# Kernel optimization log

Measured on AMD Instinct MI355X. Metric: run time of the kernel, lower is better.

The kernel has to match this reference:

```python
import jax, jax.numpy as jnp
import numpy as np

B, L, D, N = 2, 2048, 1024, 16
DT_MIN, DT_MAX = 1e-3, 1e-1


def setup_inputs() -> dict:
    key = jax.random.key(0)
    ks = jax.random.split(key, 8)
    u = jax.random.normal(ks[0], (B, L, D), dtype=jnp.float32)
    # torch.nn.Linear weights are (out_features, in_features)
    W_dt = jax.random.normal(ks[1], (D, D), dtype=jnp.float32) * 0.02
    b_dt = jnp.zeros((D,), dtype=jnp.float32)
    W_B = jax.random.normal(ks[2], (D * N, D), dtype=jnp.float32) * 0.02
    b_B = jnp.zeros((D * N,), dtype=jnp.float32)
    W_C = jax.random.normal(ks[3], (D * N, D), dtype=jnp.float32) * 0.02
    b_C = jnp.zeros((D * N,), dtype=jnp.float32)
    # log_A init: log(1..N) broadcast over channels (HiPPO-ish diagonal)
    log_A = jnp.broadcast_to(jnp.log(jnp.arange(1, N + 1, dtype=jnp.float32)), (D, N))
    D_skip = jnp.ones((D,), dtype=jnp.float32)
    lo, hi = float(np.log(DT_MIN)), float(np.log(DT_MAX))
    dt_bias = jax.random.uniform(ks[4], (D,), dtype=jnp.float32) * (hi - lo) + lo
    return {"u": u, "log_A": log_A, "D_skip": D_skip, "dt_bias": dt_bias,
            "W_dt": W_dt, "b_dt": b_dt, "W_B": W_B, "b_B": b_B,
            "W_C": W_C, "b_C": b_C}


def reference(u, log_A, D_skip, dt_bias, W_dt, b_dt, W_B, b_B, W_C, b_C):
    b, l, d = u.shape
    n = log_A.shape[1]
    A = -jnp.exp(log_A)                                   # (d, n), A < 0
    # token-dependent parameters, computed for all timesteps at once
    dt = jax.nn.softplus(u @ W_dt.T + b_dt + dt_bias)     # (b, l, d)
    Bt = (u @ W_B.T + b_B).reshape(b, l, d, n)            # (b, l, d, n)
    Ct = (u @ W_C.T + b_C).reshape(b, l, d, n)            # (b, l, d, n)
    # exact ZOH discretisation
    A_bar = jnp.exp(dt[..., None] * A)                    # (b, l, d, n)
    B_bar = (A_bar - 1.0) / A * Bt                        # (b, l, d, n)
    x_in = B_bar * u[..., None]                           # (b, l, d, n)
    # recurrent scan over time
    def step(h, inp):
        a_t, x_t, c_t = inp                               # each (b, d, n)
        h = a_t * h + x_t
        y_t = jnp.sum(c_t * h, axis=-1)                   # (b, d)
        return h, y_t
    h0 = jnp.zeros((b, d, n), dtype=u.dtype)
    xs = (jnp.moveaxis(A_bar, 1, 0), jnp.moveaxis(x_in, 1, 0), jnp.moveaxis(Ct, 1, 0))
    _, ys = jax.lax.scan(step, h0, xs)                    # ys: (l, b, d)
    y = jnp.moveaxis(ys, 0, 1) + D_skip * u               # (b, l, d)
    return y
```

## Files before the change

kernel.cpp:

```cpp
#include <hip/hip_runtime.h>
#include <hip/hip_bf16.h>
#include <stdint.h>

constexpr int Bb = 2;
constexpr int Ll = 2048;
constexpr int Dd = 1024;
constexpr int Nn = 16;
constexpr int NB = Dd * Nn;
constexpr int SL = 64;
constexpr int NCH = Bb * Dd;
constexpr int KCAT = 3 * Dd;

typedef __bf16 bf16_t;
typedef __bf16 bf16x8 __attribute__((ext_vector_type(8)));
typedef __bf16 bf16x4 __attribute__((ext_vector_type(4)));
typedef float f32x4 __attribute__((ext_vector_type(4)));

__device__ inline void gld_lds16(const void* g, void* l) {
    __builtin_amdgcn_global_load_lds(
        (const __attribute__((address_space(1))) unsigned int*)g,
        (__attribute__((address_space(3))) unsigned int*)l, 16, 0, 0);
}

__global__ __launch_bounds__(256) void cvt_bf16(const float* __restrict__ s,
                                                bf16_t* __restrict__ d, int n4) {
    int i = blockIdx.x * 256 + threadIdx.x;
    const int stride = gridDim.x * 256;
    const float4* s4 = (const float4*)s;
    bf16x4* d4 = (bf16x4*)d;
    for (; i < n4; i += stride) {
        float4 v = s4[i];
        bf16x4 o = {(bf16_t)v.x, (bf16_t)v.y, (bf16_t)v.z, (bf16_t)v.w};
        d4[i] = o;
    }
}

__global__ __launch_bounds__(256) void build_ucat(const float* __restrict__ u,
                                                  bf16_t* __restrict__ ucat,
                                                  bf16_t* __restrict__ ubf) {
    const int i = blockIdx.x * 256 + threadIdx.x;
    const int row = i >> 8;
    const int c = (i & 255) << 2;
    float4 v = ((const float4*)u)[i];
    bf16x4 hi = {(bf16_t)v.x, (bf16_t)v.y, (bf16_t)v.z, (bf16_t)v.w};
    bf16x4 lo = {(bf16_t)(v.x - (float)hi.x), (bf16_t)(v.y - (float)hi.y),
                 (bf16_t)(v.z - (float)hi.z), (bf16_t)(v.w - (float)hi.w)};
    bf16_t* r = ucat + (size_t)row * KCAT;
    *(bf16x4*)(r + c) = hi;
    *(bf16x4*)(r + Dd + c) = lo;
    *(bf16x4*)(r + 2 * Dd + c) = hi;
    *(bf16x4*)(ubf + (size_t)i * 4) = hi;
}

__global__ __launch_bounds__(256) void build_wcat(const float* __restrict__ w,
                                                  bf16_t* __restrict__ wcat) {
    const int i = blockIdx.x * 256 + threadIdx.x;
    const int row = i >> 8;
    const int c = (i & 255) << 2;
    float4 v = ((const float4*)w)[i];
    bf16x4 hi = {(bf16_t)v.x, (bf16_t)v.y, (bf16_t)v.z, (bf16_t)v.w};
    bf16x4 lo = {(bf16_t)(v.x - (float)hi.x), (bf16_t)(v.y - (float)hi.y),
                 (bf16_t)(v.z - (float)hi.z), (bf16_t)(v.w - (float)hi.w)};
    bf16_t* r = wcat + (size_t)row * KCAT;
    *(bf16x4*)(r + c) = hi;
    *(bf16x4*)(r + Dd + c) = hi;
    *(bf16x4*)(r + 2 * Dd + c) = lo;
}

template <int EP, typename OutT>
__global__ __launch_bounds__(256) void gemm_mfma(
    const bf16_t* __restrict__ Abase, int CL, int l0, int K,
    const bf16_t* __restrict__ W, const float* __restrict__ b1,
    const float* __restrict__ b2, OutT* __restrict__ C, int N)
{
    __shared__ bf16_t As[128 * 32];
    __shared__ bf16_t Bs[128 * 32];

    const int tid = threadIdx.x;
    const int bn = blockIdx.x * 128;
    const int rglob = blockIdx.y * 128;
    const int batch = rglob / CL;
    const int rin = rglob % CL;
    const bf16_t* Ap = Abase + ((size_t)batch * Ll + l0 + rin) * K;
    const bf16_t* Wp = W + (size_t)bn * K;
    OutT* Cp = C + (size_t)rglob * N;

    const int sr = tid >> 2;
    const int sc = (tid & 3) << 3;
    char* ldsA = (char*)As + tid * 16;
    char* ldsB = (char*)Bs + tid * 16;

    const int lane = tid & 63;
    const int wid = tid >> 6;
    const int wm = (wid & 1) << 6;
    const int wn = (wid >> 1) << 6;
    const int lr = lane & 15;
    const int lq = lane >> 4;

    f32x4 acc[4][4] = {};

    for (int k0 = 0; k0 < K; k0 += 32) {
        __syncthreads();
        gld_lds16(Ap + (size_t)sr * K + k0 + sc, ldsA);
        gld_lds16(Ap + (size_t)(sr + 64) * K + k0 + sc, ldsA + 4096);
        gld_lds16(Wp + (size_t)sr * K + k0 + sc, ldsB);
        gld_lds16(Wp + (size_t)(sr + 64) * K + k0 + sc, ldsB + 4096);
        __syncthreads();

        bf16x8 af[4], bfr[4];
#pragma unroll
        for (int mi = 0; mi < 4; ++mi)
            af[mi] = *(const bf16x8*)&As[(wm + mi * 16 + lr) * 32 + lq * 8];
#pragma unroll
        for (int ni = 0; ni < 4; ++ni)
            bfr[ni] = *(const bf16x8*)&Bs[(wn + ni * 16 + lr) * 32 + lq * 8];
#pragma unroll
        for (int mi = 0; mi < 4; ++mi)
#pragma unroll
            for (int ni = 0; ni < 4; ++ni)
                acc[mi][ni] = __builtin_amdgcn_mfma_f32_16x16x32_bf16(
                    af[mi], bfr[ni], acc[mi][ni], 0, 0, 0);
    }

#pragma unroll
    for (int ni = 0; ni < 4; ++ni) {
        const int col = bn + wn + ni * 16 + lr;
        const float bc = b1[col] + (EP == 1 ? b2[col] : 0.f);
#pragma unroll
        for (int mi = 0; mi < 4; ++mi)
#pragma unroll
            for (int i = 0; i < 4; ++i) {
                float v = acc[mi][ni][i] + bc;
                if (EP == 1) v = (v > 20.f) ? v : log1pf(__expf(v));
                Cp[(size_t)(wm + mi * 16 + lq * 4 + i) * N + col] = (OutT)v;
            }
    }
}

__global__ __launch_bounds__(512, 4) void gemm_dt(
    const bf16_t* __restrict__ A, int K, const bf16_t* __restrict__ W,
    const float* __restrict__ b1, const float* __restrict__ b2,
    float* __restrict__ C)
{
    extern __shared__ char smem[];
    char* const smA = smem;
    char* const smB = smem + 49152;
    const int tid = threadIdx.x;
    const int bn = blockIdx.x * 128;
    const int row0 = blockIdx.y * 128;
    const bf16_t* Ap = A + (size_t)row0 * K;
    const bf16_t* Wp = W + (size_t)bn * K;
    float* Cp = C + (size_t)row0 * Dd;

    const int lane = tid & 63;
    const int wid = tid >> 6;
    const int wr = wid >> 2;
    const int wc = wid & 3;
    const int lr = lane & 15;
    const int lq = lane >> 4;
    const int NT = K >> 6;

    const int c0 = tid, c1 = tid + 512;
    const int r0 = c0 >> 3, r1 = c1 >> 3;
    const int kb0 = ((c0 & 7) << 3) ^ ((r0 & 7) << 3);
    const int kb1 = ((c1 & 7) << 3) ^ ((r1 & 7) << 3);

    auto stageA = [&](int tt, int slot) {
        gld_lds16(Ap + (size_t)r0 * K + tt * 64 + kb0, smA + slot * 16384 + c0 * 16);
        gld_lds16(Ap + (size_t)r1 * K + tt * 64 + kb1, smA + slot * 16384 + c1 * 16);
    };
    auto stageB = [&](int tt, int slot) {
        gld_lds16(Wp + (size_t)r0 * K + tt * 64 + kb0, smB + slot * 16384 + c0 * 16);
        gld_lds16(Wp + (size_t)r1 * K + tt * 64 + kb1, smB + slot * 16384 + c1 * 16);
    };

    stageA(0, 0); stageB(0, 0); stageA(1, 1); stageB(1, 1);
    asm volatile("s_waitcnt vmcnt(4)" ::: "memory");
    __builtin_amdgcn_s_barrier();

    f32x4 acc[4][2] = {};
    const int xsw = (lr & 7) << 4;
    int as_rd = 0, as_wr = 2;

    for (int t = 0; t < NT; ++t) {
        const char* Ard = smA + as_rd * 16384;
        const char* Brd = smB + (t & 1) * 16384;

        bf16x8 bfr[2][2];
#pragma unroll
        for (int p = 0; p < 4; ++p) {
            if (p == 0 && t + 2 < NT) stageA(t + 2, as_wr);
            if (p == 2 && t + 2 < NT) stageB(t + 2, (t & 1));

            if (p == 0) {
#pragma unroll
                for (int ks = 0; ks < 2; ++ks)
#pragma unroll
                    for (int ni = 0; ni < 2; ++ni)
                        bfr[ks][ni] = *(const bf16x8*)(Brd +
                            (wc * 32 + ni * 16 + lr) * 128 +
                            ((ks * 64 + lq * 16) ^ xsw));
            }
            bf16x8 ak0 = *(const bf16x8*)(Ard +
                (wr * 64 + p * 16 + lr) * 128 + ((lq * 16) ^ xsw));
            bf16x8 ak1 = *(const bf16x8*)(Ard +
                (wr * 64 + p * 16 + lr) * 128 + ((64 + lq * 16) ^ xsw));

            __builtin_amdgcn_s_barrier();
            __builtin_amdgcn_s_setprio(1);
#pragma unroll
            for (int ni = 0; ni < 2; ++ni) {
                acc[p][ni] = __builtin_amdgcn_mfma_f32_16x16x32_bf16(
                    bfr[0][ni], ak0, acc[p][ni], 0, 0, 0);
                acc[p][ni] = __builtin_amdgcn_mfma_f32_16x16x32_bf16(
                    bfr[1][ni], ak1, acc[p][ni], 0, 0, 0);
            }
            __builtin_amdgcn_s_setprio(0);
            if (p == 3) {
                if (t + 2 < NT)
                    asm volatile("s_waitcnt vmcnt(4)" ::: "memory");
                else if (t + 1 < NT)
                    asm volatile("s_waitcnt vmcnt(0)" ::: "memory");
            }
            __builtin_amdgcn_s_barrier();
        }
        ++as_rd; if (as_rd == 3) as_rd = 0;
        ++as_wr; if (as_wr == 3) as_wr = 0;
    }

#pragma unroll
    for (int ni = 0; ni < 2; ++ni) {
        const int col = bn + wc * 32 + ni * 16 + lq * 4;
        const float4 ba = *(const float4*)&b1[col];
        const float4 bb = *(const float4*)&b2[col];
        const float bc[4] = {ba.x + bb.x, ba.y + bb.y, ba.z + bb.z, ba.w + bb.w};
#pragma unroll
        for (int mi = 0; mi < 4; ++mi) {
            const int row = wr * 64 + mi * 16 + lr;
            f32x4 v;
#pragma unroll
            for (int i = 0; i < 4; ++i) {
                float tv = acc[mi][ni][i] + bc[i];
                v[i] = (tv > 20.f) ? tv : log1pf(__expf(tv));
            }
            *(f32x4*)(Cp + (size_t)row * Dd + col) = v;
        }
    }
}

__global__ __launch_bounds__(512, 2) void gemm256_bc(
    const bf16_t* __restrict__ Abase, int CL, int l0, int K,
    const bf16_t* __restrict__ WB, const bf16_t* __restrict__ WC,
    const float* __restrict__ bB, const float* __restrict__ bC,
    bf16_t* __restrict__ OB, bf16_t* __restrict__ OC)
{
    extern __shared__ char smem[];
    char* const smA = smem;
    char* const smB = smem + 98304;
    const int tid = threadIdx.x;

    const int NY = (2 * CL) >> 8;
    const int id = blockIdx.x;
    const int cx = id & 7;
    const int jj = id >> 3;
    const int x = cx * 16 + jj / NY;
    const int yb = jj % NY;

    const int rglob = yb * 256;
    const int batch = rglob / CL;
    const int rin = rglob % CL;
    const bf16_t* Ap = Abase + ((size_t)batch * Ll + l0 + rin) * K;

    const bf16_t* Wp; const float* bias; bf16_t* Co; int bn;
    if (x < 64) { Wp = WB; bias = bB; Co = OB; bn = x * 256; }
    else        { Wp = WC; bias = bC; Co = OC; bn = (x - 64) * 256; }
    Wp += (size_t)bn * K;
    bf16_t* Cp = Co + (size_t)rglob * NB;

    const int lane = tid & 63;
    const int wid = tid >> 6;
    const int wr = wid >> 2;
    const int wc = wid & 3;
    const int lr = lane & 15;
    const int lq = lane >> 4;
    const int NT = K >> 6;

    const int c0 = tid, c1 = tid + 512;
    const int r0 = c0 >> 3, r1 = c1 >> 3;
    const int kb0 = ((c0 & 7) << 3) ^ ((r0 & 7) << 3);
    const int kb1 = ((c1 & 7) << 3) ^ ((r1 & 7) << 3);

    auto stageA = [&](int tt, int slot, int h) {
        gld_lds16(Ap + (size_t)(h * 128 + r0) * K + tt * 64 + kb0,
                  smA + slot * 32768 + h * 16384 + c0 * 16);
        gld_lds16(Ap + (size_t)(h * 128 + r1) * K + tt * 64 + kb1,
                  smA + slot * 32768 + h * 16384 + c1 * 16);
    };
    auto stageB = [&](int tt, int slot, int h) {
        gld_lds16(Wp + (size_t)(h * 128 + r0) * K + tt * 64 + kb0,
                  smB + slot * 32768 + h * 16384 + c0 * 16);
        gld_lds16(Wp + (size_t)(h * 128 + r1) * K + tt * 64 + kb1,
                  smB + slot * 32768 + h * 16384 + c1 * 16);
    };

    stageB(0, 0, 0); stageB(0, 0, 1);
    stageA(0, 0, 0); stageA(0, 0, 1);
    stageA(1, 1, 0); stageA(1, 1, 1);
    asm volatile("s_waitcnt vmcnt(4)" ::: "memory");
    __builtin_amdgcn_s_barrier();

    f32x4 acc[8][4] = {};
    const int xsw = (lr & 7) << 4;
    int as_rd = 0, as_wr = 2;

    for (int t = 0; t < NT; ++t) {
        const char* Ard = smA + as_rd * 32768;
        const char* Brd = smB + (t & 1) * 32768;

        if (t + 1 < NT) { stageB(t + 1, (t + 1) & 1, 0); stageB(t + 1, (t + 1) & 1, 1); }
        if (t + 2 < NT) { stageA(t + 2, as_wr, 0); stageA(t + 2, as_wr, 1); }

        bf16x8 bfr[2][4];
#pragma unroll
        for (int ks = 0; ks < 2; ++ks)
#pragma unroll
            for (int ni = 0; ni < 4; ++ni)
                bfr[ks][ni] = *(const bf16x8*)(Brd +
                    (wc * 64 + ni * 16 + lr) * 128 +
                    ((ks * 64 + lq * 16) ^ xsw));

#pragma unroll
        for (int p = 0; p < 4; ++p) {
            bf16x8 a0k0 = *(const bf16x8*)(Ard +
                (wr * 128 + (2 * p) * 16 + lr) * 128 + ((lq * 16) ^ xsw));
            bf16x8 a0k1 = *(const bf16x8*)(Ard +
                (wr * 128 + (2 * p) * 16 + lr) * 128 + ((64 + lq * 16) ^ xsw));
            bf16x8 a1k0 = *(const bf16x8*)(Ard +
                (wr * 128 + (2 * p + 1) * 16 + lr) * 128 + ((lq * 16) ^ xsw));
            bf16x8 a1k1 = *(const bf16x8*)(Ard +
                (wr * 128 + (2 * p + 1) * 16 + lr) * 128 + ((64 + lq * 16) ^ xsw));
#pragma unroll
            for (int ni = 0; ni < 4; ++ni) {
                acc[2 * p][ni] = __builtin_amdgcn_mfma_f32_16x16x32_bf16(
                    bfr[0][ni], a0k0, acc[2 * p][ni], 0, 0, 0);
                acc[2 * p][ni] = __builtin_amdgcn_mfma_f32_16x16x32_bf16(
                    bfr[1][ni], a0k1, acc[2 * p][ni], 0, 0, 0);
                acc[2 * p + 1][ni] = __builtin_amdgcn_mfma_f32_16x16x32_bf16(
                    bfr[0][ni], a1k0, acc[2 * p + 1][ni], 0, 0, 0);
                acc[2 * p + 1][ni] = __builtin_amdgcn_mfma_f32_16x16x32_bf16(
                    bfr[1][ni], a1k1, acc[2 * p + 1][ni], 0, 0, 0);
            }
        }

        if (t + 2 < NT)
            asm volatile("s_waitcnt vmcnt(4)" ::: "memory");
        else if (t + 1 < NT)
            asm volatile("s_waitcnt vmcnt(0)" ::: "memory");
        __builtin_amdgcn_s_barrier();

        ++as_rd; if (as_rd == 3) as_rd = 0;
        ++as_wr; if (as_wr == 3) as_wr = 0;
    }

    float4 bv[4];
#pragma unroll
    for (int ni = 0; ni < 4; ++ni)
        bv[ni] = *(const float4*)&bias[bn + wc * 64 + ni * 16 + lq * 4];
#pragma unroll
    for (int mi = 0; mi < 8; ++mi) {
        const size_t rowoff = (size_t)(wr * 128 + mi * 16 + lr) * NB;
#pragma unroll
        for (int ni = 0; ni < 4; ++ni) {
            const int col = bn + wc * 64 + ni * 16 + lq * 4;
            bf16x4 o = {(bf16_t)(acc[mi][ni][0] + bv[ni].x),
                        (bf16_t)(acc[mi][ni][1] + bv[ni].y),
                        (bf16_t)(acc[mi][ni][2] + bv[ni].z),
                        (bf16_t)(acc[mi][ni][3] + bv[ni].w)};
            *(bf16x4*)(Cp + rowoff + col) = o;
        }
    }
}

__global__ __launch_bounds__(256) void scan_seg_local(
    const float* __restrict__ u, const float* __restrict__ dt,
    const bf16_t* __restrict__ Bt_c, const float* __restrict__ log_A,
    float* __restrict__ pseg, float* __restrict__ hseg, int CL, int l0)
{
    const int tid = threadIdx.x;
    const int g = tid >> 4, n = tid & 15;
    const int gid = blockIdx.x * 16 + g;
    const int ch = gid & (NCH - 1);
    const int s = gid >> 11;
    const int b = ch >> 10, d = ch & (Dd - 1);

    const float A = -__expf(log_A[d * Nn + n]);
    const float rA = 1.f / A;

    size_t idx_bn = (size_t)(b * CL + s * SL) * NB + d * Nn + n;
    size_t idx_u = ((size_t)b * Ll + l0 + s * SL) * Dd + d;

    float p = 1.f, h = 0.f;
    for (int l = 0; l < SL; ++l) {
        const float dtv = dt[idx_u];
        const float uv = u[idx_u];
        const float bv = (float)Bt_c[idx_bn];
        const float a = __expf(dtv * A);
        p *= a;
        h = a * h + (a - 1.f) * rA * bv * uv;
        idx_bn += NB; idx_u += Dd;
    }
    const size_t o = ((size_t)s * NCH + ch) * Nn + n;
    pseg[o] = p;
    hseg[o] = h;
}

__global__ __launch_bounds__(256) void scan_combine(
    const float* __restrict__ pseg, const float* __restrict__ hseg,
    float* __restrict__ hin_arr, float* __restrict__ h_state,
    int NSEG, int l0)
{
    const int t = blockIdx.x * 256 + threadIdx.x;
    float hin = (l0 == 0) ? 0.f : h_state[t];
    for (int s = 0; s < NSEG; ++s) {
        const size_t o = (size_t)s * (NCH * Nn) + t;
        hin_arr[o] = hin;
        hin = pseg[o] * hin + hseg[o];
    }
    h_state[t] = hin;
}

__global__ __launch_bounds__(256) void scan_seg_final(
    const float* __restrict__ u, const float* __restrict__ dt,
    const bf16_t* __restrict__ Bt_c, const bf16_t* __restrict__ Ct_c,
    const float* __restrict__ log_A, const float* __restrict__ D_skip,
    const float* __restrict__ hin_arr, float* __restrict__ y, int CL, int l0)
{
    const int tid = threadIdx.x;
    const int g = tid >> 4, n = tid & 15;
    const int gid = blockIdx.x * 16 + g;
    const int ch = gid & (NCH - 1);
    const int s = gid >> 11;
    const int b = ch >> 10, d = ch & (Dd - 1);

    const float A = -__expf(log_A[d * Nn + n]);
    const float rA = 1.f / A;
    const float Dsk = D_skip[d];

    size_t idx_bn = (size_t)(b * CL + s * SL) * NB + d * Nn + n;
    size_t idx_u = ((size_t)b * Ll + l0 + s * SL) * Dd + d;

    float h = hin_arr[((size_t)s * NCH + ch) * Nn + n];
    for (int l = 0; l < SL; ++l) {
        const float dtv = dt[idx_u];
        const float uv = u[idx_u];
        const float bv = (float)Bt_c[idx_bn];
        const float cv = (float)Ct_c[idx_bn];
        const float a = __expf(dtv * A);
        h = a * h + (a - 1.f) * rA * bv * uv;
        float p = cv * h;
        p += __shfl_xor(p, 1);
        p += __shfl_xor(p, 2);
        p += __shfl_xor(p, 4);
        p += __shfl_xor(p, 8);
        if (n == 0) y[idx_u] = p + Dsk * uv;
        idx_bn += NB; idx_u += Dd;
    }
}

static inline size_t al256(size_t x) { return (x + 255) & ~(size_t)255; }

extern "C" void kernel_launch(void* const* d_in, const int* in_sizes, int n_in,
                              void* d_out, int out_size, void* d_ws, size_t ws_size,
                              hipStream_t stream) {
    const float* u       = (const float*)d_in[0];
    const float* log_A   = (const float*)d_in[1];
    const float* D_skip  = (const float*)d_in[2];
    const float* dt_bias = (const float*)d_in[3];
    const float* W_dt    = (const float*)d_in[4];
    const float* b_dt    = (const float*)d_in[5];
    const float* W_B     = (const float*)d_in[6];
    const float* b_B     = (const float*)d_in[7];
    const float* W_C     = (const float*)d_in[8];
    const float* b_C     = (const float*)d_in[9];
    float* y = (float*)d_out;

    hipFuncSetAttribute(reinterpret_cast<const void*>(gemm256_bc),
                        hipFuncAttributeMaxDynamicSharedMemorySize, 163840);
    hipFuncSetAttribute(reinterpret_cast<const void*>(gemm_dt),
                        hipFuncAttributeMaxDynamicSharedMemorySize, 81920);

    const size_t sz_ubf  = al256((size_t)Bb * Ll * Dd * 2);
    const size_t sz_w    = al256((size_t)NB * Dd * 2);
    const size_t sz_h    = al256((size_t)NCH * Nn * 4);
    const size_t sz_dtf  = al256((size_t)Bb * Ll * Dd * 4);
    const size_t sz_ucat = al256((size_t)Bb * Ll * KCAT * 2);
    const size_t sz_wcat = al256((size_t)Dd * KCAT * 2);

    int CL = 128;
    const int cands[5] = {2048, 1024, 512, 256, 128};
    for (int i = 0; i < 5; ++i) {
        const int c = cands[i];
        const int nseg = c / SL;
        const size_t seg = 3 * al256((size_t)nseg * NCH * Nn * 4);
        const size_t chunk = 2 * al256((size_t)2 * c * NB * 2);
        const size_t ovl = sz_ucat + sz_wcat;
        const size_t need = sz_ubf + 2 * sz_w + sz_h + sz_dtf + seg +
                            (chunk > ovl ? chunk : ovl);
        if (need <= ws_size) { CL = c; break; }
    }
    const int NSEG = CL / SL;

    char* p = (char*)d_ws;
    bf16_t* u_bf   = (bf16_t*)p; p += sz_ubf;
    bf16_t* wB_bf  = (bf16_t*)p; p += sz_w;
    bf16_t* wC_bf  = (bf16_t*)p; p += sz_w;
    float* h_state = (float*)p; p += sz_h;
    float* dt_full = (float*)p; p += sz_dtf;
    const size_t sz_seg1 = al256((size_t)NSEG * NCH * Nn * 4);
    float* pseg    = (float*)p; p += sz_seg1;
    float* hseg    = (float*)p; p += sz_seg1;
    float* hin_arr = (float*)p; p += sz_seg1;
    char* chunk0 = p;
    bf16_t* Bt_c = (bf16_t*)chunk0;
    bf16_t* Ct_c = (bf16_t*)(chunk0 + al256((size_t)2 * CL * NB * 2));
    bf16_t* u_cat = (bf16_t*)chunk0;
    bf16_t* w_cat = (bf16_t*)(chunk0 + sz_ucat);

    cvt_bf16<<<2048, 256, 0, stream>>>(W_B, wB_bf, NB * Dd / 4);
    cvt_bf16<<<2048, 256, 0, stream>>>(W_C, wC_bf, NB * Dd / 4);
    build_ucat<<<Bb * Ll * Dd / 4 / 256, 256, 0, stream>>>(u, u_cat, u_bf);
    build_wcat<<<Dd * Dd / 4 / 256, 256, 0, stream>>>(W_dt, w_cat);

    gemm_dt<<<dim3(Dd / 128, Bb * Ll / 128), 512, 81920, stream>>>(
        u_cat, KCAT, w_cat, b_dt, dt_bias, dt_full);

    const bool use256 = (CL % 256 == 0);
    for (int l0 = 0; l0 < Ll; l0 += CL) {
        if (use256) {
            const int NY = 2 * CL / 256;
            gemm256_bc<<<dim3(128 * NY), 512, 163840, stream>>>(
                u_bf, CL, l0, Dd, wB_bf, wC_bf, b_B, b_C, Bt_c, Ct_c);
        } else {
            gemm_mfma<0, bf16_t><<<dim3(NB / 128, 2 * CL / 128), 256, 0, stream>>>(
                u_bf, CL, l0, Dd, wB_bf, b_B, nullptr, Bt_c, NB);
            gemm_mfma<0, bf16_t><<<dim3(NB / 128, 2 * CL / 128), 256, 0, stream>>>(
                u_bf, CL, l0, Dd, wC_bf, b_C, nullptr, Ct_c, NB);
        }
        scan_seg_local<<<dim3(128 * NSEG), 256, 0, stream>>>(
            u, dt_full, Bt_c, log_A, pseg, hseg, CL, l0);
        scan_combine<<<dim3(128), 256, 0, stream>>>(
            pseg, hseg, hin_arr, h_state, NSEG, l0);
        scan_seg_final<<<dim3(128 * NSEG), 256, 0, stream>>>(
            u, dt_full, Bt_c, Ct_c, log_A, D_skip, hin_arr, y, CL, l0);
    }
}
```

Before: 686.1 us.

## Fuse prep kernels, switch B/C GEMM to 32x32 MFMA, fold scan combine into final

Merges the four bf16 conversion and concat kernels into one grid-stride prep kernel to cut launch count. Rewrites the inner loop of the 256-tile B/C GEMM to use 32x32x16 bf16 MFMA instructions with fewer fragment loads per K step. It also removes the separate scan_combine kernel: each final-scan block recomputes its incoming state by serially chaining the earlier segment summaries, with a ping-pong h_state buffer across chunks. The trade is redundant prefix work per segment in exchange for fewer launches and less intermediate memory.

After: 709.9 us. 3.5% more time.

```diff
diff --git a/kernel.cpp b/kernel.cpp
--- a/kernel.cpp
+++ b/kernel.cpp
@@ -15,6 +15,7 @@
 typedef __bf16 bf16x8 __attribute__((ext_vector_type(8)));
 typedef __bf16 bf16x4 __attribute__((ext_vector_type(4)));
 typedef float f32x4 __attribute__((ext_vector_type(4)));
+typedef float f32x16 __attribute__((ext_vector_type(16)));
 
 __device__ inline void gld_lds16(const void* g, void* l) {
     __builtin_amdgcn_global_load_lds(
@@ -22,49 +23,53 @@
         (__attribute__((address_space(3))) unsigned int*)l, 16, 0, 0);
 }
 
-__global__ __launch_bounds__(256) void cvt_bf16(const float* __restrict__ s,
-                                                bf16_t* __restrict__ d, int n4) {
+__global__ __launch_bounds__(256) void prep_all(
+    const float* __restrict__ u, const float* __restrict__ W_B,
+    const float* __restrict__ W_C, const float* __restrict__ W_dt,
+    bf16_t* __restrict__ wB_bf, bf16_t* __restrict__ wC_bf,
+    bf16_t* __restrict__ ucat, bf16_t* __restrict__ ubf,
+    bf16_t* __restrict__ wcat)
+{
+    constexpr int NW = NB * Dd / 4;
+    constexpr int NU = Bb * Ll * Dd / 4;
+    constexpr int NWc = Dd * Dd / 4;
+    constexpr int TOT = 2 * NW + NU + NWc;
     int i = blockIdx.x * 256 + threadIdx.x;
     const int stride = gridDim.x * 256;
-    const float4* s4 = (const float4*)s;
-    bf16x4* d4 = (bf16x4*)d;
-    for (; i < n4; i += stride) {
-        float4 v = s4[i];
-        bf16x4 o = {(bf16_t)v.x, (bf16_t)v.y, (bf16_t)v.z, (bf16_t)v.w};
-        d4[i] = o;
-    }
-}
-
-__global__ __launch_bounds__(256) void build_ucat(const float* __restrict__ u,
-                                                  bf16_t* __restrict__ ucat,
-                                                  bf16_t* __restrict__ ubf) {
-    const int i = blockIdx.x * 256 + threadIdx.x;
-    const int row = i >> 8;
-    const int c = (i & 255) << 2;
-    float4 v = ((const float4*)u)[i];
-    bf16x4 hi = {(bf16_t)v.x, (bf16_t)v.y, (bf16_t)v.z, (bf16_t)v.w};
-    bf16x4 lo = {(bf16_t)(v.x - (float)hi.x), (bf16_t)(v.y - (float)hi.y),
-                 (bf16_t)(v.z - (float)hi.z), (bf16_t)(v.w - (float)hi.w)};
-    bf16_t* r = ucat + (size_t)row * KCAT;
-    *(bf16x4*)(r + c) = hi;
-    *(bf16x4*)(r + Dd + c) = lo;
-    *(bf16x4*)(r + 2 * Dd + c) = hi;
-    *(bf16x4*)(ubf + (size_t)i * 4) = hi;
-}
-
-__global__ __launch_bounds__(256) void build_wcat(const float* __restrict__ w,
-                                                  bf16_t* __restrict__ wcat) {
-    const int i = blockIdx.x * 256 + threadIdx.x;
-    const int row = i >> 8;
-    const int c = (i & 255) << 2;
-    float4 v = ((const float4*)w)[i];
-    bf16x4 hi = {(bf16_t)v.x, (bf16_t)v.y, (bf16_t)v.z, (bf16_t)v.w};
-    bf16x4 lo = {(bf16_t)(v.x - (float)hi.x), (bf16_t)(v.y - (float)hi.y),
-                 (bf16_t)(v.z - (float)hi.z), (bf16_t)(v.w - (float)hi.w)};
-    bf16_t* r = wcat + (size_t)row * KCAT;
-    *(bf16x4*)(r + c) = hi;
-    *(bf16x4*)(r + Dd + c) = hi;
-    *(bf16x4*)(r + 2 * Dd + c) = lo;
+    for (; i < TOT; i += stride) {
+        if (i < 2 * NW) {
+            const float4 v = (i < NW) ? ((const float4*)W_B)[i]
+                                      : ((const float4*)W_C)[i - NW];
+            bf16x4 o = {(bf16_t)v.x, (bf16_t)v.y, (bf16_t)v.z, (bf16_t)v.w};
+            if (i < NW) ((bf16x4*)wB_bf)[i] = o;
+            else        ((bf16x4*)wC_bf)[i - NW] = o;
+        } else if (i < 2 * NW + NU) {
+            const int j = i - 2 * NW;
+            const int row = j >> 8;
+            const int c = (j & 255) << 2;
+            float4 v = ((const float4*)u)[j];
+            bf16x4 hi = {(bf16_t)v.x, (bf16_t)v.y, (bf16_t)v.z, (bf16_t)v.w};
+            bf16x4 lo = {(bf16_t)(v.x - (float)hi.x), (bf16_t)(v.y - (float)hi.y),
+                         (bf16_t)(v.z - (float)hi.z), (bf16_t)(v.w - (float)hi.w)};
+            bf16_t* r = ucat + (size_t)row * KCAT;
+            *(bf16x4*)(r + c) = hi;
+            *(bf16x4*)(r + Dd + c) = lo;
+            *(bf16x4*)(r + 2 * Dd + c) = hi;
+            *(bf16x4*)(ubf + (size_t)j * 4) = hi;
+        } else {
+            const int j = i - 2 * NW - NU;
+            const int row = j >> 8;
+            const int c = (j & 255) << 2;
+            float4 v = ((const float4*)W_dt)[j];
+            bf16x4 hi = {(bf16_t)v.x, (bf16_t)v.y, (bf16_t)v.z, (bf16_t)v.w};
+            bf16x4 lo = {(bf16_t)(v.x - (float)hi.x), (bf16_t)(v.y - (float)hi.y),
+                         (bf16_t)(v.z - (float)hi.z), (bf16_t)(v.w - (float)hi.w)};
+            bf16_t* r = wcat + (size_t)row * KCAT;
+            *(bf16x4*)(r + c) = hi;
+            *(bf16x4*)(r + Dd + c) = hi;
+            *(bf16x4*)(r + 2 * Dd + c) = lo;
+        }
+    }
 }
 
 template <int EP, typename OutT>
@@ -281,8 +286,8 @@
     const int wid = tid >> 6;
     const int wr = wid >> 2;
     const int wc = wid & 3;
-    const int lr = lane & 15;
-    const int lq = lane >> 4;
+    const int lr5 = lane & 31;
+    const int hq = lane >> 5;
     const int NT = K >> 6;
 
     const int c0 = tid, c1 = tid + 512;
@@ -309,9 +314,11 @@
     asm volatile("s_waitcnt vmcnt(4)" ::: "memory");
     __builtin_amdgcn_s_barrier();
 
-    f32x4 acc[8][4] = {};
-    const int xsw = (lr & 7) << 4;
+    f32x16 acc[4][2] = {};
     int as_rd = 0, as_wr = 2;
+
+    const int arow = wr * 128 + lr5;
+    const int brow = wc * 64 + lr5;
 
     for (int t = 0; t < NT; ++t) {
         const char* Ard = smA + as_rd * 32768;
@@ -320,36 +327,26 @@
         if (t + 1 < NT) { stageB(t + 1, (t + 1) & 1, 0); stageB(t + 1, (t + 1) & 1, 1); }
         if (t + 2 < NT) { stageA(t + 2, as_wr, 0); stageA(t + 2, as_wr, 1); }
 
-        bf16x8 bfr[2][4];
-#pragma unroll
-        for (int ks = 0; ks < 2; ++ks)
-#pragma unroll
-            for (int ni = 0; ni < 4; ++ni)
-                bfr[ks][ni] = *(const bf16x8*)(Brd +
-                    (wc * 64 + ni * 16 + lr) * 128 +
-                    ((ks * 64 + lq * 16) ^ xsw));
-
-#pragma unroll
-        for (int p = 0; p < 4; ++p) {
-            bf16x8 a0k0 = *(const bf16x8*)(Ard +
-                (wr * 128 + (2 * p) * 16 + lr) * 128 + ((lq * 16) ^ xsw));
-            bf16x8 a0k1 = *(const bf16x8*)(Ard +
-                (wr * 128 + (2 * p) * 16 + lr) * 128 + ((64 + lq * 16) ^ xsw));
-            bf16x8 a1k0 = *(const bf16x8*)(Ard +
-                (wr * 128 + (2 * p + 1) * 16 + lr) * 128 + ((lq * 16) ^ xsw));
-            bf16x8 a1k1 = *(const bf16x8*)(Ard +
-                (wr * 128 + (2 * p + 1) * 16 + lr) * 128 + ((64 + lq * 16) ^ xsw));
-#pragma unroll
-            for (int ni = 0; ni < 4; ++ni) {
-                acc[2 * p][ni] = __builtin_amdgcn_mfma_f32_16x16x32_bf16(
-                    bfr[0][ni], a0k0, acc[2 * p][ni], 0, 0, 0);
-                acc[2 * p][ni] = __builtin_amdgcn_mfma_f32_16x16x32_bf16(
-                    bfr[1][ni], a0k1, acc[2 * p][ni], 0, 0, 0);
-                acc[2 * p + 1][ni] = __builtin_amdgcn_mfma_f32_16x16x32_bf16(
-                    bfr[0][ni], a1k0, acc[2 * p + 1][ni], 0, 0, 0);
-                acc[2 * p + 1][ni] = __builtin_amdgcn_mfma_f32_16x16x32_bf16(
-                    bfr[1][ni], a1k1, acc[2 * p + 1][ni], 0, 0, 0);
-            }
+#pragma unroll
+        for (int ks = 0; ks < 4; ++ks) {
+            const int kb = ks * 32 + hq * 16;
+            bf16x8 bfr[2], afr[4];
+#pragma unroll
+            for (int ni = 0; ni < 2; ++ni) {
+                const int row = brow + ni * 32;
+                bfr[ni] = *(const bf16x8*)(Brd + row * 128 + (kb ^ ((row & 7) << 4)));
+            }
+#pragma unroll
+            for (int mi = 0; mi < 4; ++mi) {
+                const int row = arow + mi * 32;
+                afr[mi] = *(const bf16x8*)(Ard + row * 128 + (kb ^ ((row & 7) << 4)));
+            }
+#pragma unroll
+            for (int mi = 0; mi < 4; ++mi)
+#pragma unroll
+                for (int ni = 0; ni < 2; ++ni)
+                    acc[mi][ni] = __builtin_amdgcn_mfma_f32_32x32x16_bf16(
+                        bfr[ni], afr[mi], acc[mi][ni], 0, 0, 0);
         }
 
         if (t + 2 < NT)
@@ -362,21 +359,26 @@
         ++as_wr; if (as_wr == 3) as_wr = 0;
     }
 
-    float4 bv[4];
-#pragma unroll
-    for (int ni = 0; ni < 4; ++ni)
-        bv[ni] = *(const float4*)&bias[bn + wc * 64 + ni * 16 + lq * 4];
-#pragma unroll
-    for (int mi = 0; mi < 8; ++mi) {
-        const size_t rowoff = (size_t)(wr * 128 + mi * 16 + lr) * NB;
-#pragma unroll
-        for (int ni = 0; ni < 4; ++ni) {
-            const int col = bn + wc * 64 + ni * 16 + lq * 4;
-            bf16x4 o = {(bf16_t)(acc[mi][ni][0] + bv[ni].x),
-                        (bf16_t)(acc[mi][ni][1] + bv[ni].y),
-                        (bf16_t)(acc[mi][ni][2] + bv[ni].z),
-                        (bf16_t)(acc[mi][ni][3] + bv[ni].w)};
-            *(bf16x4*)(Cp + rowoff + col) = o;
+    float4 bv[2][4];
+#pragma unroll
+    for (int ni = 0; ni < 2; ++ni)
+#pragma unroll
+        for (int j = 0; j < 4; ++j)
+            bv[ni][j] = *(const float4*)&bias[bn + wc * 64 + ni * 32 + 4 * hq + 8 * j];
+#pragma unroll
+    for (int mi = 0; mi < 4; ++mi) {
+        const size_t rowoff = (size_t)(wr * 128 + mi * 32 + lr5) * NB;
+#pragma unroll
+        for (int ni = 0; ni < 2; ++ni) {
+            const int colbase = bn + wc * 64 + ni * 32 + 4 * hq;
+#pragma unroll
+            for (int j = 0; j < 4; ++j) {
+                bf16x4 o = {(bf16_t)(acc[mi][ni][4 * j + 0] + bv[ni][j].x),
+                            (bf16_t)(acc[mi][ni][4 * j + 1] + bv[ni][j].y),
+                            (bf16_t)(acc[mi][ni][4 * j + 2] + bv[ni][j].z),
+                            (bf16_t)(acc[mi][ni][4 * j + 3] + bv[ni][j].w)};
+                *(bf16x4*)(Cp + rowoff + colbase + 8 * j) = o;
+            }
         }
     }
 }
@@ -414,26 +416,13 @@
     hseg[o] = h;
 }
 
-__global__ __launch_bounds__(256) void scan_combine(
-    const float* __restrict__ pseg, const float* __restrict__ hseg,
-    float* __restrict__ hin_arr, float* __restrict__ h_state,
-    int NSEG, int l0)
-{
-    const int t = blockIdx.x * 256 + threadIdx.x;
-    float hin = (l0 == 0) ? 0.f : h_state[t];
-    for (int s = 0; s < NSEG; ++s) {
-        const size_t o = (size_t)s * (NCH * Nn) + t;
-        hin_arr[o] = hin;
-        hin = pseg[o] * hin + hseg[o];
-    }
-    h_state[t] = hin;
-}
-
 __global__ __launch_bounds__(256) void scan_seg_final(
     const float* __restrict__ u, const float* __restrict__ dt,
     const bf16_t* __restrict__ Bt_c, const bf16_t* __restrict__ Ct_c,
     const float* __restrict__ log_A, const float* __restrict__ D_skip,
-    const float* __restrict__ hin_arr, float* __restrict__ y, int CL, int l0)
+    const float* __restrict__ pseg, const float* __restrict__ hseg,
+    const float* __restrict__ h_in, float* __restrict__ h_out,
+    float* __restrict__ y, int CL, int l0, int NSEG)
 {
     const int tid = threadIdx.x;
     const int g = tid >> 4, n = tid & 15;
@@ -446,10 +435,16 @@
     const float rA = 1.f / A;
     const float Dsk = D_skip[d];
 
+    const int t32 = ch * Nn + n;
+    float h = (l0 == 0) ? 0.f : h_in[t32];
+    for (int s2 = 0; s2 < s; ++s2) {
+        const size_t o2 = (size_t)s2 * (NCH * Nn) + t32;
+        h = pseg[o2] * h + hseg[o2];
+    }
+
     size_t idx_bn = (size_t)(b * CL + s * SL) * NB + d * Nn + n;
     size_t idx_u = ((size_t)b * Ll + l0 + s * SL) * Dd + d;
 
-    float h = hin_arr[((size_t)s * NCH + ch) * Nn + n];
     for (int l = 0; l < SL; ++l) {
         const float dtv = dt[idx_u];
         const float uv = u[idx_u];
@@ -465,6 +460,8 @@
         if (n == 0) y[idx_u] = p + Dsk * uv;
         idx_bn += NB; idx_u += Dd;
     }
+
+    if (s == NSEG - 1) h_out[t32] = h;
 }
 
 static inline size_t al256(size_t x) { return (x + 255) & ~(size_t)255; }
@@ -491,7 +488,7 @@
 
     const size_t sz_ubf  = al256((size_t)Bb * Ll * Dd * 2);
     const size_t sz_w    = al256((size_t)NB * Dd * 2);
-    const size_t sz_h    = al256((size_t)NCH * Nn * 4);
+    const size_t sz_h    = al256((size_t)NCH * Nn * 4) * 2;
     const size_t sz_dtf  = al256((size_t)Bb * Ll * Dd * 4);
     const size_t sz_ucat = al256((size_t)Bb * Ll * KCAT * 2);
     const size_t sz_wcat = al256((size_t)Dd * KCAT * 2);
@@ -501,7 +498,7 @@
     for (int i = 0; i < 5; ++i) {
         const int c = cands[i];
         const int nseg = c / SL;
-        const size_t seg = 3 * al256((size_t)nseg * NCH * Nn * 4);
+        const size_t seg = 2 * al256((size_t)nseg * NCH * Nn * 4);
         const size_t chunk = 2 * al256((size_t)2 * c * NB * 2);
         const size_t ovl = sz_ucat + sz_wcat;
         const size_t need = sz_ubf + 2 * sz_w + sz_h + sz_dtf + seg +
@@ -519,23 +516,22 @@
     const size_t sz_seg1 = al256((size_t)NSEG * NCH * Nn * 4);
     float* pseg    = (float*)p; p += sz_seg1;
     float* hseg    = (float*)p; p += sz_seg1;
-    float* hin_arr = (float*)p; p += sz_seg1;
     char* chunk0 = p;
     bf16_t* Bt_c = (bf16_t*)chunk0;
     bf16_t* Ct_c = (bf16_t*)(chunk0 + al256((size_t)2 * CL * NB * 2));
     bf16_t* u_cat = (bf16_t*)chunk0;
     bf16_t* w_cat = (bf16_t*)(chunk0 + sz_ucat);
 
-    cvt_bf16<<<2048, 256, 0, stream>>>(W_B, wB_bf, NB * Dd / 4);
-    cvt_bf16<<<2048, 256, 0, stream>>>(W_C, wC_bf, NB * Dd / 4);
-    build_ucat<<<Bb * Ll * Dd / 4 / 256, 256, 0, stream>>>(u, u_cat, u_bf);
-    build_wcat<<<Dd * Dd / 4 / 256, 256, 0, stream>>>(W_dt, w_cat);
+    prep_all<<<2048, 256, 0, stream>>>(u, W_B, W_C, W_dt,
+                                       wB_bf, wC_bf, u_cat, u_bf, w_cat);
 
     gemm_dt<<<dim3(Dd / 128, Bb * Ll / 128), 512, 81920, stream>>>(
         u_cat, KCAT, w_cat, b_dt, dt_bias, dt_full);
 
     const bool use256 = (CL % 256 == 0);
-    for (int l0 = 0; l0 < Ll; l0 += CL) {
+    const int HS = NCH * Nn;
+    int par = 0;
+    for (int l0 = 0; l0 < Ll; l0 += CL, par ^= 1) {
         if (use256) {
             const int NY = 2 * CL / 256;
             gemm256_bc<<<dim3(128 * NY), 512, 163840, stream>>>(
@@ -548,9 +544,8 @@
         }
         scan_seg_local<<<dim3(128 * NSEG), 256, 0, stream>>>(
             u, dt_full, Bt_c, log_A, pseg, hseg, CL, l0);
-        scan_combine<<<dim3(128), 256, 0, stream>>>(
-            pseg, hseg, hin_arr, h_state, NSEG, l0);
         scan_seg_final<<<dim3(128 * NSEG), 256, 0, stream>>>(
-            u, dt_full, Bt_c, Ct_c, log_A, D_skip, hin_arr, y, CL, l0);
-    }
-}
+            u, dt_full, Bt_c, Ct_c, log_A, D_skip, pseg, hseg,
+            h_state + par * HS, h_state + (par ^ 1) * HS, y, CL, l0, NSEG);
+    }
+}
```
